# Performance work log

Hardware: AMD Instinct MI355X
Metric: run time of the kernel (lower is better)

## Reference

```python
import jax, jax.numpy as jnp
import numpy as np

H = 1024

def gru_step(x, h, W_ih, W_hh, b_ih, b_hh):
    # torch.nn.GRUCell math; gate order r, z, n
    gi = x @ W_ih.T + b_ih            # [N, 3H]
    gh = h @ W_hh.T + b_hh            # [N, 3H]
    i_r, i_z, i_n = jnp.split(gi, 3, axis=-1)
    h_r, h_z, h_n = jnp.split(gh, 3, axis=-1)
    r = jax.nn.sigmoid(i_r + h_r)
    z = jax.nn.sigmoid(i_z + h_z)
    n = jnp.tanh(i_n + r * h_n)
    return (1.0 - z) * n + z * h


def setup_inputs() -> dict:
    key = jax.random.key(0)
    ks = jax.random.split(key, 12)
    V, Nr, Na = 256, 4096, 4096
    s = 1.0 / np.sqrt(H)
    return {
        'state': jax.random.normal(ks[0], (1, H), jnp.float32),
        'rel_tokens': jax.random.randint(ks[1], (Nr, 3), 0, V, jnp.int32),
        'attr_tokens': jax.random.randint(ks[2], (Na, 2), 0, V, jnp.int32),
        'table': jax.random.normal(ks[3], (V, H), jnp.float32),
        'W_emb': jax.random.normal(ks[4], (H, H), jnp.float32) * s,
        'b_emb': jnp.zeros((H,), jnp.float32),
        'W_ih': jax.random.normal(ks[5], (3 * H, H), jnp.float32) * s,
        'W_hh': jax.random.normal(ks[6], (3 * H, H), jnp.float32) * s,
        'b_ih': jnp.zeros((3 * H,), jnp.float32),
        'b_hh': jnp.zeros((3 * H,), jnp.float32),
        'W1': jax.random.normal(ks[7], (H, H), jnp.float32) * s,
        'b1': jnp.zeros((H,), jnp.float32),
        'W2': jax.random.normal(ks[8], (H, H), jnp.float32) * s,
        'b2': jnp.zeros((H,), jnp.float32),
        'W3': jax.random.normal(ks[9], (1, H), jnp.float32) * s,
        'b3': jnp.zeros((1,), jnp.float32),
        'eps': jax.random.uniform(ks[10], (1,), jnp.float32) * 0.1,
    }


def reference(state, rel_tokens, attr_tokens, table, W_emb, b_emb,
              W_ih, W_hh, b_ih, b_hh, W1, b1, W2, b2, W3, b3, eps):
    Nr, Na = rel_tokens.shape[0], attr_tokens.shape[0]
    # per-clause token embeddings passed through embedding_layer (Linear)
    rel_e = jnp.einsum('nte,he->nth', table[rel_tokens], W_emb) + b_emb   # [Nr,3,H]
    att_e = jnp.einsum('nte,he->nth', table[attr_tokens], W_emb) + b_emb  # [Na,2,H]

    # relation clauses: 3 chained GRU steps from global state
    h = jnp.broadcast_to(state, (Nr, H))
    for t in range(3):
        h = gru_step(rel_e[:, t], h, W_ih, W_hh, b_ih, b_hh)
    rel_h = h
    # attribute clauses: 2 chained GRU steps from global state
    h = jnp.broadcast_to(state, (Na, H))
    for t in range(2):
        h = gru_step(att_e[:, t], h, W_ih, W_hh, b_ih, b_hh)
    attr_h = h

    clause = jnp.concatenate([rel_h, attr_h], axis=0)          # [N, H]
    x = jax.nn.relu(clause @ W1.T + b1)
    x = jax.nn.relu(x @ W2.T + b2)
    logits = (x @ W3.T + b3).reshape(1, -1)                    # [1, N]
    probs = jax.nn.softmax(logits, axis=1)                     # softmax over clauses
    n = jnp.float32(probs.shape[1])
    probs = probs * (1.0 - eps[0]) + eps[0] / n                # eps smoothing
    return probs
```

## Files before the change

### kernel.cpp

```cpp
#include <hip/hip_runtime.h>
#include <math.h>

#define H 1024
#define H3 3072
#define NVOC 256

typedef __attribute__((ext_vector_type(8))) short bf16x8;
typedef __attribute__((ext_vector_type(4))) float f32x4;

__device__ __forceinline__ float sigf(float x) { return 1.0f / (1.0f + expf(-x)); }

__device__ __forceinline__ unsigned short f2bf(float f) {
    unsigned int u = __float_as_uint(f);
    u = (u + 0x7fffu + ((u >> 16) & 1u)) >> 16;
    return (unsigned short)u;
}
__device__ __forceinline__ float bf2f(unsigned short u) {
    return __uint_as_float(((unsigned int)u) << 16);
}

template<bool RELU, int OUT_MODE>
__global__ __launch_bounds__(256)
void gemm_bf16(const unsigned short* __restrict__ A, const unsigned short* __restrict__ W,
               const float* __restrict__ bias, void* __restrict__ C,
               int N, int K, int gx,
               const float* __restrict__ w3, float* __restrict__ logits)
{
    __shared__ unsigned short As[128 * 32];
    __shared__ unsigned short Ws[128 * 32];
    const int tid = threadIdx.x;
    const int wid = tid >> 6, lane = tid & 63;

    const int nwg = gridDim.x;
    const int cpx = nwg >> 3;
    const int bid = blockIdx.x;
    const int swz = (bid & 7) * cpx + (bid >> 3);
    const int bm = (swz / gx) * 128;
    const int bn = (swz % gx) * 128;

    const int wm = (wid >> 1) * 64, wn = (wid & 1) * 64;

    f32x4 acc[4][4];
#pragma unroll
    for (int i = 0; i < 4; i++)
#pragma unroll
        for (int j = 0; j < 4; j++) acc[i][j] = (f32x4){0.f, 0.f, 0.f, 0.f};

    const int l4 = lane >> 2;
    const int c8 = (lane & 3) * 8;
    const int fr = lane & 15;
    const int fq = lane >> 4;

    for (int k0 = 0; k0 < K; k0 += 32) {
#pragma unroll
        for (int issue = 0; issue < 2; issue++) {
            const int chunk = issue * 4 + wid;
            const int row = chunk * 16 + l4;
            const unsigned short* ga = A + (size_t)(bm + row) * K + k0 + c8;
            const unsigned short* gw = W + (size_t)(bn + row) * K + k0 + c8;
            __builtin_amdgcn_global_load_lds(
                (const __attribute__((address_space(1))) void*)ga,
                (__attribute__((address_space(3))) void*)(As + chunk * 512), 16, 0, 0);
            __builtin_amdgcn_global_load_lds(
                (const __attribute__((address_space(1))) void*)gw,
                (__attribute__((address_space(3))) void*)(Ws + chunk * 512), 16, 0, 0);
        }
        __syncthreads();

        bf16x8 a[4], b[4];
#pragma unroll
        for (int m = 0; m < 4; m++)
            a[m] = *reinterpret_cast<const bf16x8*>(As + (wm + m * 16 + fr) * 32 + fq * 8);
#pragma unroll
        for (int n = 0; n < 4; n++)
            b[n] = *reinterpret_cast<const bf16x8*>(Ws + (wn + n * 16 + fr) * 32 + fq * 8);
#pragma unroll
        for (int m = 0; m < 4; m++)
#pragma unroll
            for (int n = 0; n < 4; n++)
                acc[m][n] = __builtin_amdgcn_mfma_f32_16x16x32_bf16(a[m], b[n], acc[m][n], 0, 0, 0);
        __syncthreads();
    }

    if (OUT_MODE == 2) {
        float rs[4][4];
#pragma unroll
        for (int m = 0; m < 4; m++)
#pragma unroll
            for (int j = 0; j < 4; j++) rs[m][j] = 0.f;
#pragma unroll
        for (int n = 0; n < 4; n++) {
            const int col = bn + wn + n * 16 + fr;
            const float bv = bias[col];
            const float wv = w3[col];
#pragma unroll
            for (int m = 0; m < 4; m++)
#pragma unroll
                for (int j = 0; j < 4; j++) {
                    float v = acc[m][n][j] + bv;
                    if (RELU) v = fmaxf(v, 0.f);
                    rs[m][j] = fmaf(v, wv, rs[m][j]);
                }
        }
#pragma unroll
        for (int m = 0; m < 4; m++)
#pragma unroll
            for (int j = 0; j < 4; j++) {
                float s = rs[m][j];
                s += __shfl_xor(s, 1); s += __shfl_xor(s, 2);
                s += __shfl_xor(s, 4); s += __shfl_xor(s, 8);
                if (fr == 0) atomicAdd(logits + bm + wm + m * 16 + fq * 4 + j, s);
            }
    } else {
#pragma unroll
        for (int m = 0; m < 4; m++) {
#pragma unroll
            for (int n = 0; n < 4; n++) {
                const int col = bn + wn + n * 16 + fr;
                const float bv = bias[col];
#pragma unroll
                for (int j = 0; j < 4; j++) {
                    const int row = bm + wm + m * 16 + fq * 4 + j;
                    float v = acc[m][n][j] + bv;
                    if (RELU) v = fmaxf(v, 0.f);
                    if (OUT_MODE == 1)
                        ((unsigned short*)C)[(size_t)row * N + col] = f2bf(v);
                    else
                        ((float*)C)[(size_t)row * N + col] = v;
                }
            }
        }
    }
}

__global__ void cvt_all(const float* __restrict__ W_hh, const float* __restrict__ W_ih,
                        const float* __restrict__ W1, const float* __restrict__ W2,
                        const float* __restrict__ W_emb, const float* __restrict__ table,
                        unsigned short* __restrict__ W_hhb, unsigned short* __restrict__ W_ihb,
                        unsigned short* __restrict__ W1b, unsigned short* __restrict__ W2b,
                        unsigned short* __restrict__ W_embb, unsigned short* __restrict__ tableb)
{
    const int C1 = H3 * H, C2 = H * H, C3 = NVOC * H;
    int off = (blockIdx.x * blockDim.x + threadIdx.x) * 4;
    const float* src; unsigned short* dst;
    if (off < C1)               { src = W_hh;  dst = W_hhb; }
    else if ((off -= C1) < C1)  { src = W_ih;  dst = W_ihb; }
    else if ((off -= C1) < C2)  { src = W1;    dst = W1b; }
    else if ((off -= C2) < C2)  { src = W2;    dst = W2b; }
    else if ((off -= C2) < C2)  { src = W_emb; dst = W_embb; }
    else if ((off -= C2) < C3)  { src = table; dst = tableb; }
    else return;
    float4 v = *reinterpret_cast<const float4*>(src + off);
    ushort4 o;
    o.x = f2bf(v.x); o.y = f2bf(v.y); o.z = f2bf(v.z); o.w = f2bf(v.w);
    *reinterpret_cast<ushort4*>(dst + off) = o;
}

__global__ void gemv_bf16w(const float* __restrict__ x, const unsigned short* __restrict__ Wm,
                           const float* __restrict__ bias, float* __restrict__ out,
                           int N, int K)
{
    int wid = threadIdx.x >> 6;
    int lane = threadIdx.x & 63;
    int n = blockIdx.x * (blockDim.x >> 6) + wid;
    if (n >= N) return;
    const unsigned short* wr = Wm + (size_t)n * K;
    float s = 0.f;
    for (int p = 0; p < K; p += 256) {
        float4 xv = *reinterpret_cast<const float4*>(x + p + lane * 4);
        ushort4 wv = *reinterpret_cast<const ushort4*>(wr + p + lane * 4);
        s = fmaf(xv.x, bf2f(wv.x), s); s = fmaf(xv.y, bf2f(wv.y), s);
        s = fmaf(xv.z, bf2f(wv.z), s); s = fmaf(xv.w, bf2f(wv.w), s);
    }
#pragma unroll
    for (int off = 32; off; off >>= 1) s += __shfl_down(s, off);
    if (lane == 0) out[n] = s + (bias ? bias[n] : 0.f);
}

__global__ void h1_combine(const float* __restrict__ Gi, const float* __restrict__ gh0,
                           const float* __restrict__ state, float* __restrict__ h1,
                           unsigned short* __restrict__ h1b)
{
    int idx = blockIdx.x * blockDim.x + threadIdx.x;
    int v = idx >> 10, h = idx & (H - 1);
    const float* g = Gi + (size_t)v * H3;
    float r = sigf(g[h] + gh0[h]);
    float z = sigf(g[H + h] + gh0[H + h]);
    float n = tanhf(fmaf(r, gh0[2 * H + h], g[2 * H + h]));
    float v2 = (1.f - z) * n + z * state[h];
    h1[idx] = v2;
    h1b[idx] = f2bf(v2);
}

__global__ void step2_both(const int* __restrict__ rel, const int* __restrict__ attr, int Nr,
                           const float* __restrict__ Gi, const float* __restrict__ gh1,
                           const float* __restrict__ h1,
                           unsigned short* __restrict__ h2b, unsigned short* __restrict__ attr_out)
{
    int idx = blockIdx.x * blockDim.x + threadIdx.x;
    int row = idx >> 10, h = idx & (H - 1);
    int t0, t1, orow = row;
    unsigned short* dst;
    if (row < Nr) { t0 = rel[row * 3 + 0]; t1 = rel[row * 3 + 1]; dst = h2b; }
    else { orow = row - Nr; t0 = attr[orow * 2 + 0]; t1 = attr[orow * 2 + 1]; dst = attr_out; }
    const float* g = Gi + (size_t)t1 * H3;
    const float* gh = gh1 + (size_t)t0 * H3;
    float r = sigf(g[h] + gh[h]);
    float z = sigf(g[H + h] + gh[H + h]);
    float n = tanhf(fmaf(r, gh[2 * H + h], g[2 * H + h]));
    float v = (1.f - z) * n + z * h1[(size_t)t0 * H + h];
    dst[(size_t)orow * H + h] = f2bf(v);
}

__global__ void step3_rel(const int* __restrict__ toks,
                          const float* __restrict__ Gi, const unsigned short* __restrict__ gh2b,
                          const unsigned short* __restrict__ h2b, unsigned short* __restrict__ outb)
{
    int idx = blockIdx.x * blockDim.x + threadIdx.x;
    int row = idx >> 10, h = idx & (H - 1);
    int t2 = toks[row * 3 + 2];
    const float* g = Gi + (size_t)t2 * H3;
    const unsigned short* gh = gh2b + (size_t)row * H3;
    float r = sigf(g[h] + bf2f(gh[h]));
    float z = sigf(g[H + h] + bf2f(gh[H + h]));
    float n = tanhf(fmaf(r, bf2f(gh[2 * H + h]), g[2 * H + h]));
    outb[idx] = f2bf((1.f - z) * n + z * bf2f(h2b[idx]));
}

__global__ void softmax_eps(const float* __restrict__ logits, const float* __restrict__ epsp,
                            float* __restrict__ out, int N)
{
    __shared__ float smax[16], ssum[16];
    int tid = threadIdx.x;
    int nw = blockDim.x >> 6;
    float m = -INFINITY;
    for (int i = tid; i < N; i += blockDim.x) m = fmaxf(m, logits[i]);
#pragma unroll
    for (int off = 32; off; off >>= 1) m = fmaxf(m, __shfl_down(m, off));
    if ((tid & 63) == 0) smax[tid >> 6] = m;
    __syncthreads();
    float M = smax[0];
    for (int i = 1; i < nw; i++) M = fmaxf(M, smax[i]);
    float s = 0.f;
    for (int i = tid; i < N; i += blockDim.x) s += expf(logits[i] - M);
#pragma unroll
    for (int off = 32; off; off >>= 1) s += __shfl_down(s, off);
    if ((tid & 63) == 0) ssum[tid >> 6] = s;
    __syncthreads();
    float S = 0.f;
    for (int i = 0; i < nw; i++) S += ssum[i];
    float e = epsp[0];
    float mul = (1.f - e) / S;
    float add = e / (float)N;
    for (int i = tid; i < N; i += blockDim.x) out[i] = expf(logits[i] - M) * mul + add;
}

extern "C" void kernel_launch(void* const* d_in, const int* in_sizes, int n_in,
                              void* d_out, int out_size, void* d_ws, size_t ws_size,
                              hipStream_t stream)
{
    const float* state       = (const float*)d_in[0];
    const int*   rel_tokens  = (const int*)d_in[1];
    const int*   attr_tokens = (const int*)d_in[2];
    const float* table       = (const float*)d_in[3];
    const float* W_emb       = (const float*)d_in[4];
    const float* b_emb       = (const float*)d_in[5];
    const float* W_ih        = (const float*)d_in[6];
    const float* W_hh        = (const float*)d_in[7];
    const float* b_ih        = (const float*)d_in[8];
    const float* b_hh        = (const float*)d_in[9];
    const float* W1          = (const float*)d_in[10];
    const float* b1          = (const float*)d_in[11];
    const float* W2          = (const float*)d_in[12];
    const float* b2          = (const float*)d_in[13];
    const float* W3          = (const float*)d_in[14];
    const float* eps         = (const float*)d_in[16];

    const int Nr = in_sizes[1] / 3;
    const int Na = in_sizes[2] / 2;
    const int Ntot = Nr + Na;

    float* ws     = (float*)d_ws;
    float* Gi     = ws;
    float* gh0    = Gi + NVOC * H3;
    float* h1     = gh0 + H3;
    float* gh1    = h1 + NVOC * H;
    float* logits = gh1 + NVOC * H3;
    unsigned short* W_hhb   = (unsigned short*)(logits + Ntot);
    unsigned short* W_ihb   = W_hhb + (size_t)H3 * H;
    unsigned short* W1b     = W_ihb + (size_t)H3 * H;
    unsigned short* W2b     = W1b + (size_t)H * H;
    unsigned short* W_embb  = W2b + (size_t)H * H;
    unsigned short* tableb  = W_embb + (size_t)H * H;
    unsigned short* embb    = tableb + (size_t)NVOC * H;
    unsigned short* h1b     = embb + (size_t)NVOC * H;
    unsigned short* h2b     = h1b + (size_t)NVOC * H;
    unsigned short* gh2b    = h2b + (size_t)Nr * H;
    unsigned short* clauseb = gh2b + (size_t)Nr * H3;
    unsigned short* x1b     = clauseb + (size_t)Ntot * H;

    {
        const int total = 2 * H3 * H + 3 * H * H + NVOC * H;
        cvt_all<<<(total / 4 + 255) / 256, 256, 0, stream>>>(
            W_hh, W_ih, W1, W2, W_emb, table,
            W_hhb, W_ihb, W1b, W2b, W_embb, tableb);
    }
    hipMemsetAsync(logits, 0, Ntot * sizeof(float), stream);

    gemm_bf16<false, 1><<<(H / 128) * (NVOC / 128), 256, 0, stream>>>(
        tableb, W_embb, b_emb, embb, H, H, H / 128, nullptr, nullptr);
    gemm_bf16<false, 0><<<(H3 / 128) * (NVOC / 128), 256, 0, stream>>>(
        embb, W_ihb, b_ih, Gi, H3, H, H3 / 128, nullptr, nullptr);
    gemv_bf16w<<<H3 / 4, 256, 0, stream>>>(state, W_hhb, b_hh, gh0, H3, H);
    h1_combine<<<NVOC * H / 256, 256, 0, stream>>>(Gi, gh0, state, h1, h1b);
    gemm_bf16<false, 0><<<(H3 / 128) * (NVOC / 128), 256, 0, stream>>>(
        h1b, W_hhb, b_hh, gh1, H3, H, H3 / 128, nullptr, nullptr);
    step2_both<<<Ntot * (H / 256), 256, 0, stream>>>(rel_tokens, attr_tokens, Nr,
                                                     Gi, gh1, h1, h2b,
                                                     clauseb + (size_t)Nr * H);
    gemm_bf16<false, 1><<<(H3 / 128) * (Nr / 128), 256, 0, stream>>>(
        h2b, W_hhb, b_hh, gh2b, H3, H, H3 / 128, nullptr, nullptr);
    step3_rel<<<Nr * (H / 256), 256, 0, stream>>>(rel_tokens, Gi, gh2b, h2b, clauseb);
    gemm_bf16<true, 1><<<(H / 128) * (Ntot / 128), 256, 0, stream>>>(
        clauseb, W1b, b1, x1b, H, H, H / 128, nullptr, nullptr);
    gemm_bf16<true, 2><<<(H / 128) * (Ntot / 128), 256, 0, stream>>>(
        x1b, W2b, b2, nullptr, H, H, H / 128, W3, logits);
    softmax_eps<<<1, 1024, 0, stream>>>(logits, eps, (float*)d_out, Ntot);
}
```

Measured before the change: 337.8 us.

## Multi-stage LDS pipelining, swizzled LDS layout, and split-K for small vocab GEMMs

Rewrites the bf16 GEMM main loop as a 4-buffer, 3-deep async global_load_lds pipeline with explicit vmcnt waits and a single barrier per k-step. It also XOR-swizzles the LDS chunk layout to reduce bank conflicts and raises MFMA priority. The three small vocab-sized GEMMs (256 rows) switch to 4-way split-K with atomicAdd into bias-prefilled fp32 buffers, plus a separate bf16 convert of the embedding. The aim is to hide load latency and fill more CUs on the tiny GEMMs, at the cost of more LDS per block, atomics and extra prefill/convert kernels.

```diff
diff --git a/kernel.cpp b/kernel.cpp
--- a/kernel.cpp
+++ b/kernel.cpp
@@ -23,11 +23,11 @@
 __global__ __launch_bounds__(256)
 void gemm_bf16(const unsigned short* __restrict__ A, const unsigned short* __restrict__ W,
                const float* __restrict__ bias, void* __restrict__ C,
-               int N, int K, int gx,
+               int N, int K, int gx, int Kc,
                const float* __restrict__ w3, float* __restrict__ logits)
 {
-    __shared__ unsigned short As[128 * 32];
-    __shared__ unsigned short Ws[128 * 32];
+    __shared__ unsigned short As[4][128 * 32];
+    __shared__ unsigned short Ws[4][128 * 32];
     const int tid = threadIdx.x;
     const int wid = tid >> 6, lane = tid & 63;
 
@@ -37,49 +37,71 @@
     const int swz = (bid & 7) * cpx + (bid >> 3);
     const int bm = (swz / gx) * 128;
     const int bn = (swz % gx) * 128;
+    const int k_base = blockIdx.y * Kc;
+    const int nt = Kc >> 5;
 
     const int wm = (wid >> 1) * 64, wn = (wid & 1) * 64;
-
-    f32x4 acc[4][4];
-#pragma unroll
-    for (int i = 0; i < 4; i++)
-#pragma unroll
-        for (int j = 0; j < 4; j++) acc[i][j] = (f32x4){0.f, 0.f, 0.f, 0.f};
-
-    const int l4 = lane >> 2;
-    const int c8 = (lane & 3) * 8;
     const int fr = lane & 15;
     const int fq = lane >> 4;
-
-    for (int k0 = 0; k0 < K; k0 += 32) {
-#pragma unroll
-        for (int issue = 0; issue < 2; issue++) {
-            const int chunk = issue * 4 + wid;
-            const int row = chunk * 16 + l4;
-            const unsigned short* ga = A + (size_t)(bm + row) * K + k0 + c8;
-            const unsigned short* gw = W + (size_t)(bn + row) * K + k0 + c8;
-            __builtin_amdgcn_global_load_lds(
-                (const __attribute__((address_space(1))) void*)ga,
-                (__attribute__((address_space(3))) void*)(As + chunk * 512), 16, 0, 0);
-            __builtin_amdgcn_global_load_lds(
-                (const __attribute__((address_space(1))) void*)gw,
-                (__attribute__((address_space(3))) void*)(Ws + chunk * 512), 16, 0, 0);
-        }
-        __syncthreads();
-
+    const int perm = fq ^ (fr & 3);
+
+    f32x4 acc[4][4];
+#pragma unroll
+    for (int i = 0; i < 4; i++)
+#pragma unroll
+        for (int j = 0; j < 4; j++) acc[i][j] = (f32x4){0.f, 0.f, 0.f, 0.f};
+
+    const int srow = tid >> 2;
+    const int schunk = (tid & 3) ^ (srow & 3);
+    const unsigned short* aS = A + (size_t)(bm + srow) * K + k_base + schunk * 8;
+    const unsigned short* wS = W + (size_t)(bn + srow) * K + k_base + schunk * 8;
+    const size_t rstep = (size_t)64 * K;
+
+    auto stage = [&](int b, int t) {
+        const unsigned short* a0 = aS + t * 32;
+        const unsigned short* w0 = wS + t * 32;
+        __builtin_amdgcn_global_load_lds(
+            (const __attribute__((address_space(1))) void*)a0,
+            (__attribute__((address_space(3))) void*)(&As[b][wid * 512]), 16, 0, 0);
+        __builtin_amdgcn_global_load_lds(
+            (const __attribute__((address_space(1))) void*)(a0 + rstep),
+            (__attribute__((address_space(3))) void*)(&As[b][2048 + wid * 512]), 16, 0, 0);
+        __builtin_amdgcn_global_load_lds(
+            (const __attribute__((address_space(1))) void*)w0,
+            (__attribute__((address_space(3))) void*)(&Ws[b][wid * 512]), 16, 0, 0);
+        __builtin_amdgcn_global_load_lds(
+            (const __attribute__((address_space(1))) void*)(w0 + rstep),
+            (__attribute__((address_space(3))) void*)(&Ws[b][2048 + wid * 512]), 16, 0, 0);
+    };
+
+    stage(0, 0);
+    if (nt > 1) stage(1, 1);
+    if (nt > 2) stage(2, 2);
+
+    for (int t = 0; t < nt; ++t) {
+        if (t + 2 < nt)      asm volatile("s_waitcnt vmcnt(8)" ::: "memory");
+        else if (t + 1 < nt) asm volatile("s_waitcnt vmcnt(4)" ::: "memory");
+        else                 asm volatile("s_waitcnt vmcnt(0)" ::: "memory");
+        __builtin_amdgcn_s_barrier();
+        __builtin_amdgcn_sched_barrier(0);
+        if (t + 3 < nt) stage((t + 3) & 3, t + 3);
+
+        const unsigned short* as = &As[t & 3][0];
+        const unsigned short* ws = &Ws[t & 3][0];
         bf16x8 a[4], b[4];
 #pragma unroll
         for (int m = 0; m < 4; m++)
-            a[m] = *reinterpret_cast<const bf16x8*>(As + (wm + m * 16 + fr) * 32 + fq * 8);
+            a[m] = *reinterpret_cast<const bf16x8*>(as + (wm + m * 16 + fr) * 32 + perm * 8);
 #pragma unroll
         for (int n = 0; n < 4; n++)
-            b[n] = *reinterpret_cast<const bf16x8*>(Ws + (wn + n * 16 + fr) * 32 + fq * 8);
+            b[n] = *reinterpret_cast<const bf16x8*>(ws + (wn + n * 16 + fr) * 32 + perm * 8);
+        __builtin_amdgcn_s_setprio(1);
 #pragma unroll
         for (int m = 0; m < 4; m++)
 #pragma unroll
             for (int n = 0; n < 4; n++)
                 acc[m][n] = __builtin_amdgcn_mfma_f32_16x16x32_bf16(a[m], b[n], acc[m][n], 0, 0, 0);
-        __syncthreads();
+        __builtin_amdgcn_s_setprio(0);
     }
 
     if (OUT_MODE == 2) {
@@ -110,6 +132,19 @@
                 s += __shfl_xor(s, 1); s += __shfl_xor(s, 2);
                 s += __shfl_xor(s, 4); s += __shfl_xor(s, 8);
                 if (fr == 0) atomicAdd(logits + bm + wm + m * 16 + fq * 4 + j, s);
+            }
+    } else if (OUT_MODE == 3) {
+        float* Cf = (float*)C;
+#pragma unroll
+        for (int m = 0; m < 4; m++)
+#pragma unroll
+            for (int n = 0; n < 4; n++) {
+                const int col = bn + wn + n * 16 + fr;
+#pragma unroll
+                for (int j = 0; j < 4; j++) {
+                    const int row = bm + wm + m * 16 + fq * 4 + j;
+                    atomicAdd(Cf + (size_t)row * N + col, acc[m][n][j]);
+                }
             }
     } else {
 #pragma unroll
@@ -154,6 +189,28 @@
     ushort4 o;
     o.x = f2bf(v.x); o.y = f2bf(v.y); o.z = f2bf(v.z); o.w = f2bf(v.w);
     *reinterpret_cast<ushort4*>(dst + off) = o;
+}
+
+__global__ void prefill(const float* __restrict__ b_emb, const float* __restrict__ b_ih,
+                        const float* __restrict__ b_hh,
+                        float* __restrict__ emb32, float* __restrict__ Gi,
+                        float* __restrict__ gh1, float* __restrict__ logits, int Ntot)
+{
+    const int E = NVOC * H, G = NVOC * H3;
+    int i = blockIdx.x * blockDim.x + threadIdx.x;
+    if (i < E)                { emb32[i] = b_emb[i & (H - 1)]; return; }
+    if ((i -= E) < G)         { Gi[i] = b_ih[i % H3]; return; }
+    if ((i -= G) < G)         { gh1[i] = b_hh[i % H3]; return; }
+    if ((i -= G) < Ntot)      logits[i] = 0.f;
+}
+
+__global__ void cvt_emb(const float* __restrict__ in, unsigned short* __restrict__ out)
+{
+    int i = (blockIdx.x * blockDim.x + threadIdx.x) * 4;
+    float4 v = *reinterpret_cast<const float4*>(in + i);
+    ushort4 o;
+    o.x = f2bf(v.x); o.y = f2bf(v.y); o.z = f2bf(v.z); o.w = f2bf(v.w);
+    *reinterpret_cast<ushort4*>(out + i) = o;
 }
 
 __global__ void gemv_bf16w(const float* __restrict__ x, const unsigned short* __restrict__ Wm,
@@ -285,7 +342,8 @@
     float* gh0    = Gi + NVOC * H3;
     float* h1     = gh0 + H3;
     float* gh1    = h1 + NVOC * H;
-    float* logits = gh1 + NVOC * H3;
+    float* emb32  = gh1 + NVOC * H3;
+    float* logits = emb32 + NVOC * H;
     unsigned short* W_hhb   = (unsigned short*)(logits + Ntot);
     unsigned short* W_ihb   = W_hhb + (size_t)H3 * H;
     unsigned short* W1b     = W_ihb + (size_t)H3 * H;
@@ -304,26 +362,29 @@
         cvt_all<<<(total / 4 + 255) / 256, 256, 0, stream>>>(
             W_hh, W_ih, W1, W2, W_emb, table,
             W_hhb, W_ihb, W1b, W2b, W_embb, tableb);
+        const int pf = NVOC * H + 2 * NVOC * H3 + Ntot;
+        prefill<<<(pf + 255) / 256, 256, 0, stream>>>(b_emb, b_ih, b_hh,
+                                                      emb32, Gi, gh1, logits, Ntot);
     }
-    hipMemsetAsync(logits, 0, Ntot * sizeof(float), stream);
-
-    gemm_bf16<false, 1><<<(H / 128) * (NVOC / 128), 256, 0, stream>>>(
-        tableb, W_embb, b_emb, embb, H, H, H / 128, nullptr, nullptr);
-    gemm_bf16<false, 0><<<(H3 / 128) * (NVOC / 128), 256, 0, stream>>>(
-        embb, W_ihb, b_ih, Gi, H3, H, H3 / 128, nullptr, nullptr);
+
+    gemm_bf16<false, 3><<<dim3((H / 128) * (NVOC / 128), 4), 256, 0, stream>>>(
+        tableb, W_embb, nullptr, emb32, H, H, H / 128, H / 4, nullptr, nullptr);
+    cvt_emb<<<NVOC * H / 4 / 256, 256, 0, stream>>>(emb32, embb);
+    gemm_bf16<false, 3><<<dim3((H3 / 128) * (NVOC / 128), 4), 256, 0, stream>>>(
+        embb, W_ihb, nullptr, Gi, H3, H, H3 / 128, H / 4, nullptr, nullptr);
     gemv_bf16w<<<H3 / 4, 256, 0, stream>>>(state, W_hhb, b_hh, gh0, H3, H);
     h1_combine<<<NVOC * H / 256, 256, 0, stream>>>(Gi, gh0, state, h1, h1b);
-    gemm_bf16<false, 0><<<(H3 / 128) * (NVOC / 128), 256, 0, stream>>>(
-        h1b, W_hhb, b_hh, gh1, H3, H, H3 / 128, nullptr, nullptr);
+    gemm_bf16<false, 3><<<dim3((H3 / 128) * (NVOC / 128), 4), 256, 0, stream>>>(
+        h1b, W_hhb, nullptr, gh1, H3, H, H3 / 128, H / 4, nullptr, nullptr);
     step2_both<<<Ntot * (H / 256), 256, 0, stream>>>(rel_tokens, attr_tokens, Nr,
                                                      Gi, gh1, h1, h2b,
                                                      clauseb + (size_t)Nr * H);
-    gemm_bf16<false, 1><<<(H3 / 128) * (Nr / 128), 256, 0, stream>>>(
-        h2b, W_hhb, b_hh, gh2b, H3, H, H3 / 128, nullptr, nullptr);
+    gemm_bf16<false, 1><<<dim3((H3 / 128) * (Nr / 128), 1), 256, 0, stream>>>(
+        h2b, W_hhb, b_hh, gh2b, H3, H, H3 / 128, H, nullptr, nullptr);
     step3_rel<<<Nr * (H / 256), 256, 0, stream>>>(rel_tokens, Gi, gh2b, h2b, clauseb);
-    gemm_bf16<true, 1><<<(H / 128) * (Ntot / 128), 256, 0, stream>>>(
-        clauseb, W1b, b1, x1b, H, H, H / 128, nullptr, nullptr);
-    gemm_bf16<true, 2><<<(H / 128) * (Ntot / 128), 256, 0, stream>>>(
-        x1b, W2b, b2, nullptr, H, H, H / 128, W3, logits);
+    gemm_bf16<true, 1><<<dim3((H / 128) * (Ntot / 128), 1), 256, 0, stream>>>(
+        clauseb, W1b, b1, x1b, H, H, H / 128, H, nullptr, nullptr);
+    gemm_bf16<true, 2><<<dim3((H / 128) * (Ntot / 128), 1), 256, 0, stream>>>(
+        x1b, W2b, b2, nullptr, H, H, H / 128, H, W3, logits);
     softmax_eps<<<1, 1024, 0, stream>>>(logits, eps, (float*)d_out, Ntot);
 }
```

Result: faster. 319.1 us (-5.5%).
